# Kernel tuning notes

Hardware: AMD Instinct MI355X
Metric: run time of the kernel (lower is better)

Reference implementation:

```python
import jax, jax.numpy as jnp
import numpy as np

BN_EPS = 1e-5
L2_EPS = 1e-12
REG = 10.0      # 'reg' inside ProxRefinement.forward
LAMBDA = 0.1    # Softshrink lambd (reg=0.1 in ProxRefinement.__init__)
STEPS = 10
LR = 0.01


def _softshrink(x, lam):
    return jnp.where(x > lam, x - lam, jnp.where(x < -lam, x + lam, jnp.zeros_like(x)))


def _batched_graphsage(x, adj, W, b, gamma, beta):
    # x: [B,N,F_in], adj: [B,N,N], W: [F_out,F_in]
    h = jnp.einsum('bnm,bmf->bnf', adj, x)            # neighborhood aggregate
    h = jnp.einsum('bnf,of->bno', h, W) + b           # Linear
    norm = jnp.linalg.norm(h, axis=2, keepdims=True)  # F.normalize(dim=2, p=2)
    h = h / jnp.maximum(norm, L2_EPS)
    h = jax.nn.relu(h)
    # BatchNorm1d(num_features=N) in training mode: stats over (batch, feature)
    mu = h.mean(axis=(0, 2))
    var = h.var(axis=(0, 2))
    h = (h - mu[None, :, None]) / jnp.sqrt(var[None, :, None] + BN_EPS)
    return h * gamma[None, :, None] + beta[None, :, None]


def _prox_refine(s, lap):
    s0 = s

    def body(_, s):
        grad = (jnp.einsum('bmn,bmk->bnk', lap, s)   # lap^T @ s
                + jnp.einsum('bnm,bmk->bnk', lap, s)  # lap @ s
                - REG * 2.0 * (s0 - s))
        return _softshrink(s - LR * grad, LAMBDA)

    return jax.lax.fori_loop(0, STEPS, body, s)


def setup_inputs() -> dict:
    key = jax.random.key(0)
    ks = jax.random.split(key, 6)
    B, N, nfeat, nnext = 8, 2048, 256, 512
    nhid = nfeat // 2
    x = jax.random.normal(ks[0], (B, N, nfeat), dtype=jnp.float32)
    adj = jax.random.uniform(ks[1], (B, N, N), dtype=jnp.float32)
    W1 = jax.random.normal(ks[2], (nhid, nfeat), dtype=jnp.float32) * (1.0 / np.sqrt(nfeat))
    b1 = jnp.zeros((nhid,), dtype=jnp.float32)
    g1 = jnp.ones((N,), dtype=jnp.float32)
    be1 = jnp.zeros((N,), dtype=jnp.float32)
    W2 = jax.random.normal(ks[3], (nnext, nhid), dtype=jnp.float32) * (1.0 / np.sqrt(nhid))
    b2 = jnp.zeros((nnext,), dtype=jnp.float32)
    g2 = jnp.ones((N,), dtype=jnp.float32)
    be2 = jnp.zeros((N,), dtype=jnp.float32)
    return {"x": x, "adj": adj, "W1": W1, "b1": b1, "g1": g1, "be1": be1,
            "W2": W2, "b2": b2, "g2": g2, "be2": be2}


def reference(x, adj, W1, b1, g1, be1, W2, b2, g2, be2):
    s = _batched_graphsage(x, adj, W1, b1, g1, be1)   # [B,N,nhid]
    s = _batched_graphsage(s, adj, W2, b2, g2, be2)   # [B,N,nnext]
    # Laplacian L = diag(rowsum(adj)) - adj, vectorized over batch
    deg = adj.sum(axis=-1)                             # [B,N]
    N = adj.shape[1]
    lap = deg[:, :, None] * jnp.eye(N, dtype=adj.dtype)[None] - adj
    s = _prox_refine(s, lap)
    return jax.nn.softmax(s, axis=-1)
```

## Files before the change

### kernel.cpp

```cpp
#include <hip/hip_runtime.h>
#include <cstdint>
#include <cstddef>

#define NN 2048
#define NB 8
#define F0C 256
#define F1C 128
#define F2C 512

typedef double f64x4 __attribute__((ext_vector_type(4)));

__device__ __forceinline__ double waveSumD(double v) {
#pragma unroll
    for (int o = 32; o; o >>= 1) v += __shfl_down(v, o, 64);
    return v;
}

__global__ __launch_bounds__(256) void deg_k(const float* __restrict__ adj,
                                             double* __restrict__ degD) {
    const size_t row = blockIdx.x;
    const float4* r4 = (const float4*)(adj + row * (size_t)NN);
    float4 a = r4[threadIdx.x];
    float4 b = r4[threadIdx.x + 256];
    double s = (((double)a.x + a.y) + ((double)a.z + a.w)) +
               (((double)b.x + b.y) + ((double)b.z + b.w));
    s = waveSumD(s);
    __shared__ double red[4];
    if (!(threadIdx.x & 63)) red[threadIdx.x >> 6] = s;
    __syncthreads();
    if (!threadIdx.x) degD[row] = (red[0] + red[1]) + (red[2] + red[3]);
}

template <typename BT, typename CT, bool ADD_AT, int EPI>
__global__ __launch_bounds__(256, 2) void mf_k(
    const float* __restrict__ A, size_t Abatch, int lda,
    const BT* __restrict__ Bm, size_t Bbatch, int ldb,
    CT* __restrict__ Cout, size_t Cbatch, int K, int Ccols,
    const float* __restrict__ S0, size_t Sbatch,
    const double* __restrict__ degD) {
    __shared__ float As[128][20];
    __shared__ float AsT[ADD_AT ? 16 : 1][136];
    __shared__ BT Bs[16][132];
    __shared__ double degL[EPI == 2 ? 128 : 1];

    const int b = blockIdx.z;
    const int i0 = blockIdx.x * 128;
    const int j0 = blockIdx.y * 128;
    const float* Ab = A + Abatch * (size_t)b;
    const BT* Bb = Bm + Bbatch * (size_t)b;
    const int t = threadIdx.x;
    const int l = t & 63;
    const int wv = t >> 6;
    const int wr = (wv >> 1) * 64;
    const int wc = (wv & 1) * 64;
    const int lr = l & 15;
    const int lk = l >> 4;

    f64x4 acc[4][4];
#pragma unroll
    for (int r = 0; r < 4; ++r)
#pragma unroll
        for (int c = 0; c < 4; ++c)
#pragma unroll
            for (int v = 0; v < 4; ++v) acc[r][c][v] = 0.0;

    if (EPI == 2) {
        if (t < 128) degL[t] = degD[(size_t)b * NN + i0 + t];
    }

    for (int k0 = 0; k0 < K; k0 += 16) {
        if (k0) __syncthreads();
#pragma unroll
        for (int r2 = 0; r2 < 2; ++r2) {
            const int p = t + 256 * r2;
            const int i = p >> 2, q = p & 3;
            float4 v = *(const float4*)(Ab + (size_t)(i0 + i) * lda + k0 + q * 4);
            *(float4*)&As[i][q * 4] = v;
        }
        if (ADD_AT) {
#pragma unroll
            for (int r2 = 0; r2 < 2; ++r2) {
                const int p = t + 256 * r2;
                const int k = p >> 5, c = (p & 31) * 4;
                float4 v = *(const float4*)(Ab + (size_t)(k0 + k) * lda + i0 + c);
                *(float4*)&AsT[k][c] = v;
            }
        }
        if constexpr (sizeof(BT) == 8) {
#pragma unroll
            for (int r2 = 0; r2 < 2; ++r2) {
                const int p = t + 256 * r2;
                const int k = p >> 5, c = (p & 31) * 4;
                const BT* src = Bb + (size_t)(k0 + k) * ldb + j0 + c;
                double2 u0 = *(const double2*)src;
                double2 u1 = *(const double2*)(src + 2);
                *(double2*)&Bs[k][c] = u0;
                *(double2*)&Bs[k][c + 2] = u1;
            }
        } else {
#pragma unroll
            for (int r2 = 0; r2 < 2; ++r2) {
                const int p = t + 256 * r2;
                const int k = p >> 5, c = (p & 31) * 4;
                float4 v = *(const float4*)(Bb + (size_t)(k0 + k) * ldb + j0 + c);
                Bs[k][c + 0] = (BT)v.x; Bs[k][c + 1] = (BT)v.y;
                Bs[k][c + 2] = (BT)v.z; Bs[k][c + 3] = (BT)v.w;
            }
        }
        __syncthreads();
#pragma unroll
        for (int kk = 0; kk < 4; ++kk) {
            const int kr = kk * 4 + lk;
            double av[4], bv[4];
#pragma unroll
            for (int r = 0; r < 4; ++r) {
                const int ii = wr + r * 16 + lr;
                double a = (double)As[ii][kr];
                if (ADD_AT) a += (double)AsT[kr][ii];
                av[r] = a;
            }
#pragma unroll
            for (int c = 0; c < 4; ++c)
                bv[c] = (double)Bs[kr][wc + c * 16 + lr];
#pragma unroll
            for (int r = 0; r < 4; ++r)
#pragma unroll
                for (int c = 0; c < 4; ++c)
                    acc[r][c] = __builtin_amdgcn_mfma_f64_16x16x4f64(
                        av[r], bv[c], acc[r][c], 0, 0, 0);
        }
    }

#pragma unroll
    for (int r = 0; r < 4; ++r) {
#pragma unroll
        for (int v = 0; v < 4; ++v) {
            const int rl = wr + r * 16 + lk + 4 * v;
            const size_t grow = (size_t)(i0 + rl);
            double cA = 0.0;
            if (EPI == 2) cA = 0.8 - 0.02 * degL[rl];
#pragma unroll
            for (int c = 0; c < 4; ++c) {
                const int gcol = j0 + wc + c * 16 + lr;
                double y = acc[r][c][v];
                if (EPI == 2) {
                    const double sv = (double)Bb[grow * (size_t)ldb + gcol];
                    const double s0v =
                        (double)S0[Sbatch * (size_t)b + grow * (size_t)Ccols + gcol];
                    const double u = cA * sv + 0.01 * y + 0.2 * s0v;
                    y = (u > 0.1) ? (u - 0.1) : ((u < -0.1) ? (u + 0.1) : 0.0);
                }
                Cout[Cbatch * (size_t)b + grow * (size_t)Ccols + gcol] = (CT)y;
            }
        }
    }
}

template <typename BT, typename CT>
__global__ __launch_bounds__(256) void gemm64_k(
    const float* __restrict__ A, size_t Abatch, int lda,
    const BT* __restrict__ Bm, size_t Bbatch, int ldb,
    CT* __restrict__ Cout, size_t Cbatch,
    int K, int Ccols,
    const float* __restrict__ bias,
    const float* __restrict__ S0, size_t Sbatch,
    int addAT, int btrans, int epi) {
    __shared__ float As[32][132];
    __shared__ float AsT[32][132];
    __shared__ BT Bs[32][68];
    __shared__ double degLDS[2][128];
    const int b = blockIdx.z;
    const int i0 = blockIdx.x * 128;
    const int j0 = blockIdx.y * 64;
    const float* Ab = A + Abatch * (size_t)b;
    const BT* Bb = Bm + Bbatch * (size_t)b;
    const int t = threadIdx.x;
    const int wv = t >> 6, ln = t & 63;
    const int ri = (wv >> 1) * 64 + (ln >> 3) * 8;
    const int rj = ((wv & 1) * 8 + (ln & 7)) * 4;

    double acc[8][4];
#pragma unroll
    for (int i = 0; i < 8; ++i)
#pragma unroll
        for (int j = 0; j < 4; ++j) acc[i][j] = 0.0;

    const int a_i = t >> 1, a_m = (t & 1) * 16;
    const int p_m = t >> 3, p_i = (t & 7) * 16;
    const int b_m = t >> 3, b_j = (t & 7) * 8;
    const int w_j = t >> 2, w_m = (t & 3) * 8;
    double degacc = 0.0;

    for (int k0 = 0; k0 < K; k0 += 32) {
        if (k0) __syncthreads();
        {
            const float4* src =
                (const float4*)(Ab + (size_t)(i0 + a_i) * lda + k0 + a_m);
            float4 v0 = src[0], v1 = src[1], v2 = src[2], v3 = src[3];
            if (epi == 2)
                degacc += (((double)v0.x + v0.y) + ((double)v0.z + v0.w)) +
                          (((double)v1.x + v1.y) + ((double)v1.z + v1.w)) +
                          (((double)v2.x + v2.y) + ((double)v2.z + v2.w)) +
                          (((double)v3.x + v3.y) + ((double)v3.z + v3.w));
            As[a_m + 0][a_i] = v0.x;  As[a_m + 1][a_i] = v0.y;
            As[a_m + 2][a_i] = v0.z;  As[a_m + 3][a_i] = v0.w;
            As[a_m + 4][a_i] = v1.x;  As[a_m + 5][a_i] = v1.y;
            As[a_m + 6][a_i] = v1.z;  As[a_m + 7][a_i] = v1.w;
            As[a_m + 8][a_i] = v2.x;  As[a_m + 9][a_i] = v2.y;
            As[a_m + 10][a_i] = v2.z; As[a_m + 11][a_i] = v2.w;
            As[a_m + 12][a_i] = v3.x; As[a_m + 13][a_i] = v3.y;
            As[a_m + 14][a_i] = v3.z; As[a_m + 15][a_i] = v3.w;
        }
        if (addAT) {
            const float4* src =
                (const float4*)(Ab + (size_t)(k0 + p_m) * lda + i0 + p_i);
            float4 v0 = src[0], v1 = src[1], v2 = src[2], v3 = src[3];
            AsT[p_m][p_i + 0] = v0.x;  AsT[p_m][p_i + 1] = v0.y;
            AsT[p_m][p_i + 2] = v0.z;  AsT[p_m][p_i + 3] = v0.w;
            AsT[p_m][p_i + 4] = v1.x;  AsT[p_m][p_i + 5] = v1.y;
            AsT[p_m][p_i + 6] = v1.z;  AsT[p_m][p_i + 7] = v1.w;
            AsT[p_m][p_i + 8] = v2.x;  AsT[p_m][p_i + 9] = v2.y;
            AsT[p_m][p_i + 10] = v2.z; AsT[p_m][p_i + 11] = v2.w;
            AsT[p_m][p_i + 12] = v3.x; AsT[p_m][p_i + 13] = v3.y;
            AsT[p_m][p_i + 14] = v3.z; AsT[p_m][p_i + 15] = v3.w;
        }
        if (!btrans) {
            const BT* src = Bb + (size_t)(k0 + b_m) * ldb + j0 + b_j;
            if constexpr (sizeof(BT) == 8) {
                const double2* s2 = (const double2*)src;
                double2 u0 = s2[0], u1 = s2[1], u2 = s2[2], u3 = s2[3];
                Bs[b_m][b_j + 0] = (BT)u0.x; Bs[b_m][b_j + 1] = (BT)u0.y;
                Bs[b_m][b_j + 2] = (BT)u1.x; Bs[b_m][b_j + 3] = (BT)u1.y;
                Bs[b_m][b_j + 4] = (BT)u2.x; Bs[b_m][b_j + 5] = (BT)u2.y;
                Bs[b_m][b_j + 6] = (BT)u3.x; Bs[b_m][b_j + 7] = (BT)u3.y;
            } else {
                const float4* s4 = (const float4*)src;
                float4 u0 = s4[0], u1 = s4[1];
                Bs[b_m][b_j + 0] = (BT)u0.x; Bs[b_m][b_j + 1] = (BT)u0.y;
                Bs[b_m][b_j + 2] = (BT)u0.z; Bs[b_m][b_j + 3] = (BT)u0.w;
                Bs[b_m][b_j + 4] = (BT)u1.x; Bs[b_m][b_j + 5] = (BT)u1.y;
                Bs[b_m][b_j + 6] = (BT)u1.z; Bs[b_m][b_j + 7] = (BT)u1.w;
            }
        } else {
            const float* Wf = reinterpret_cast<const float*>(Bm);
            const float4* src =
                (const float4*)(Wf + (size_t)(j0 + w_j) * ldb + k0 + w_m);
            float4 v0 = src[0], v1 = src[1];
            Bs[w_m + 0][w_j] = (BT)v0.x; Bs[w_m + 1][w_j] = (BT)v0.y;
            Bs[w_m + 2][w_j] = (BT)v0.z; Bs[w_m + 3][w_j] = (BT)v0.w;
            Bs[w_m + 4][w_j] = (BT)v1.x; Bs[w_m + 5][w_j] = (BT)v1.y;
            Bs[w_m + 6][w_j] = (BT)v1.z; Bs[w_m + 7][w_j] = (BT)v1.w;
        }
        __syncthreads();
#pragma unroll 4
        for (int mk = 0; mk < 32; ++mk) {
            float4 a0 = *(const float4*)&As[mk][ri];
            float4 a1 = *(const float4*)&As[mk][ri + 4];
            double ad[8] = {a0.x, a0.y, a0.z, a0.w, a1.x, a1.y, a1.z, a1.w};
            if (addAT) {
                float4 t0 = *(const float4*)&AsT[mk][ri];
                float4 t1 = *(const float4*)&AsT[mk][ri + 4];
                ad[0] += t0.x; ad[1] += t0.y; ad[2] += t0.z; ad[3] += t0.w;
                ad[4] += t1.x; ad[5] += t1.y; ad[6] += t1.z; ad[7] += t1.w;
            }
            double bd[4];
#pragma unroll
            for (int c = 0; c < 4; ++c) bd[c] = (double)Bs[mk][rj + c];
#pragma unroll
            for (int iy = 0; iy < 8; ++iy)
#pragma unroll
                for (int jx = 0; jx < 4; ++jx)
                    acc[iy][jx] = fma(ad[iy], bd[jx], acc[iy][jx]);
        }
    }

    if (epi == 2) degLDS[t & 1][t >> 1] = degacc;
    __syncthreads();

#pragma unroll
    for (int iy = 0; iy < 8; ++iy) {
        const int row = i0 + ri + iy;
        CT* cp = Cout + Cbatch * (size_t)b + (size_t)row * Ccols + j0 + rj;
        CT o[4];
        if (epi == 0) {
#pragma unroll
            for (int jx = 0; jx < 4; ++jx) o[jx] = (CT)acc[iy][jx];
        } else if (epi == 1) {
#pragma unroll
            for (int jx = 0; jx < 4; ++jx)
                o[jx] = (CT)(acc[iy][jx] + (double)bias[j0 + rj + jx]);
        } else {
            const double dg = degLDS[0][ri + iy] + degLDS[1][ri + iy];
            const double cA = 0.8 - 0.02 * dg;
            const BT* sp = Bb + (size_t)row * ldb + j0 + rj;
            const float* s0p = S0 + Sbatch * (size_t)b + (size_t)row * Ccols + j0 + rj;
#pragma unroll
            for (int jx = 0; jx < 4; ++jx) {
                const double u = cA * (double)sp[jx] + 0.01 * acc[iy][jx] +
                                 0.2 * (double)s0p[jx];
                const double v = (u > 0.1) ? (u - 0.1) : ((u < -0.1) ? (u + 0.1) : 0.0);
                o[jx] = (CT)v;
            }
        }
        if constexpr (sizeof(CT) == 8) {
            double2 q0, q1;
            q0.x = o[0]; q0.y = o[1]; q1.x = o[2]; q1.y = o[3];
            *(double2*)cp = q0;
            *(double2*)(cp + 2) = q1;
        } else {
            *(float4*)cp = make_float4(o[0], o[1], o[2], o[3]);
        }
    }
}

__global__ __launch_bounds__(64) void l2relu_k(float* __restrict__ buf, int F) {
    const size_t row = blockIdx.x;
    float* p = buf + row * (size_t)F;
    double ss = 0.0;
    for (int k = threadIdx.x; k < F; k += 64) {
        const double v = (double)p[k];
        ss += v * v;
    }
#pragma unroll
    for (int o = 32; o; o >>= 1) ss += __shfl_xor(ss, o, 64);
    const double den = fmax(sqrt(ss), 1e-12);
    for (int k = threadIdx.x; k < F; k += 64) {
        const double v = (double)p[k] / den;
        p[k] = (float)(v > 0.0 ? v : 0.0);
    }
}

__global__ __launch_bounds__(256) void bn_k(float* __restrict__ buf,
                                            const float* __restrict__ g,
                                            const float* __restrict__ be, int fl) {
    const int n = blockIdx.x;
    const int F = 1 << fl;
    const int total = NB << fl;
    __shared__ double red[4];
    __shared__ double sh_m, sh_scale, sh_be;
    const int wv = threadIdx.x >> 6, ln = threadIdx.x & 63;
    double s = 0.0;
    for (int idx = threadIdx.x; idx < total; idx += 256) {
        const int bb = idx >> fl, f = idx & (F - 1);
        s += (double)buf[((size_t)bb * NN + n) * F + f];
    }
    s = waveSumD(s);
    if (!ln) red[wv] = s;
    __syncthreads();
    if (!threadIdx.x) sh_m = ((red[0] + red[1]) + (red[2] + red[3])) / (double)total;
    __syncthreads();
    const double m = sh_m;
    double v2 = 0.0;
    for (int idx = threadIdx.x; idx < total; idx += 256) {
        const int bb = idx >> fl, f = idx & (F - 1);
        const double d = (double)buf[((size_t)bb * NN + n) * F + f] - m;
        v2 += d * d;
    }
    v2 = waveSumD(v2);
    __syncthreads();
    if (!ln) red[wv] = v2;
    __syncthreads();
    if (!threadIdx.x) {
        const double var = ((red[0] + red[1]) + (red[2] + red[3])) / (double)total;
        sh_scale = (1.0 / sqrt(var + 1e-5)) * (double)g[n];
        sh_be = (double)be[n];
    }
    __syncthreads();
    const double sc = sh_scale, bb2 = sh_be;
    for (int idx = threadIdx.x; idx < total; idx += 256) {
        const int bb = idx >> fl, f = idx & (F - 1);
        float* pp = &buf[((size_t)bb * NN + n) * F + f];
        *pp = (float)(((double)*pp - m) * sc + bb2);
    }
}

template <typename T>
__global__ __launch_bounds__(256) void softmax_k(const T* __restrict__ in,
                                                 float* __restrict__ out) {
    const size_t row = blockIdx.x;
    const T* p = in + row * (size_t)F2C;
    float* q = out + row * (size_t)F2C;
    const int t = threadIdx.x;
    const int wv = t >> 6, ln = t & 63;
    const double v0 = (double)p[t], v1 = (double)p[t + 256];
    double m = fmax(v0, v1);
#pragma unroll
    for (int o = 32; o; o >>= 1) m = fmax(m, __shfl_xor(m, o, 64));
    __shared__ double red[4];
    if (!ln) red[wv] = m;
    __syncthreads();
    m = fmax(fmax(red[0], red[1]), fmax(red[2], red[3]));
    const double e0 = exp(v0 - m), e1 = exp(v1 - m);
    double s = e0 + e1;
#pragma unroll
    for (int o = 32; o; o >>= 1) s += __shfl_xor(s, o, 64);
    __syncthreads();
    if (!ln) red[wv] = s;
    __syncthreads();
    s = (red[0] + red[1]) + (red[2] + red[3]);
    q[t] = (float)(e0 / s);
    q[t + 256] = (float)(e1 / s);
}

extern "C" void kernel_launch(void* const* d_in, const int* in_sizes, int n_in,
                              void* d_out, int out_size, void* d_ws, size_t ws_size,
                              hipStream_t stream) {
    const float* x = (const float*)d_in[0];
    const float* adj = (const float*)d_in[1];
    const float* W1 = (const float*)d_in[2];
    const float* b1 = (const float*)d_in[3];
    const float* g1 = (const float*)d_in[4];
    const float* be1 = (const float*)d_in[5];
    const float* W2 = (const float*)d_in[6];
    const float* b2 = (const float*)d_in[7];
    const float* g2 = (const float*)d_in[8];
    const float* be2 = (const float*)d_in[9];
    float* out = (float*)d_out;
    float* ws = (float*)d_ws;

    const size_t M2 = (size_t)NB * NN * F2C;
    const size_t szAgg = (size_t)NB * NN * F0C;

    const int tier = (ws_size >= ((size_t)192 << 20)) ? 0
                   : (ws_size >= ((size_t)64 << 20)) ? 1 : 2;

    if (tier == 0) {
        float* s0F = ws;
        float* tmpF = ws + M2;
        double* D1 = (double*)(ws + 2 * M2);
        double* D2 = D1 + M2;
        float* aggF = tmpF;
        float* t1F = tmpF + szAgg;
        float* h2F = tmpF;
        double* degD = (double*)(tmpF + 7340032);

        deg_k<<<NB * NN, 256, 0, stream>>>(adj, degD);
        mf_k<float, float, false, 0><<<dim3(16, 2, 8), 256, 0, stream>>>(
            adj, (size_t)NN * NN, NN, x, (size_t)NN * F0C, F0C,
            aggF, (size_t)NN * F0C, NN, F0C, nullptr, 0, nullptr);
        gemm64_k<float, float><<<dim3(128, 2, 1), 256, 0, stream>>>(
            aggF, 0, F0C, W1, 0, F0C, t1F, 0, F0C, F1C, b1, nullptr, 0, 0, 1, 1);
        l2relu_k<<<NB * NN, 64, 0, stream>>>(t1F, F1C);
        bn_k<<<NN, 256, 0, stream>>>(t1F, g1, be1, 7);
        mf_k<float, float, false, 0><<<dim3(16, 1, 8), 256, 0, stream>>>(
            adj, (size_t)NN * NN, NN, t1F, (size_t)NN * F1C, F1C,
            h2F, (size_t)NN * F1C, NN, F1C, nullptr, 0, nullptr);
        gemm64_k<float, float><<<dim3(128, 8, 1), 256, 0, stream>>>(
            h2F, 0, F1C, W2, 0, F1C, s0F, 0, F1C, F2C, b2, nullptr, 0, 0, 1, 1);
        l2relu_k<<<NB * NN, 64, 0, stream>>>(s0F, F2C);
        bn_k<<<NN, 256, 0, stream>>>(s0F, g2, be2, 9);
        mf_k<float, double, true, 2><<<dim3(16, 4, 8), 256, 0, stream>>>(
            adj, (size_t)NN * NN, NN, s0F, (size_t)NN * F2C, F2C,
            D1, (size_t)NN * F2C, NN, F2C, s0F, (size_t)NN * F2C, degD);
        const double* Sin = D1;
        for (int it = 1; it < 10; ++it) {
            double* Sout = (it & 1) ? D2 : D1;
            mf_k<double, double, true, 2><<<dim3(16, 4, 8), 256, 0, stream>>>(
                adj, (size_t)NN * NN, NN, Sin, (size_t)NN * F2C, F2C,
                Sout, (size_t)NN * F2C, NN, F2C, s0F, (size_t)NN * F2C, degD);
            Sin = Sout;
        }
        softmax_k<double><<<NB * NN, 256, 0, stream>>>(D2, out);
    } else if (tier == 1) {
        float* R0 = ws;
        float* R1 = ws + M2;
        float* aggF = R1;
        float* t1F = R0;
        float* h2F = R1;
        float* s0F = R0;

        gemm64_k<float, float><<<dim3(16, 4, 8), 256, 0, stream>>>(
            adj, (size_t)NN * NN, NN, x, (size_t)NN * F0C, F0C,
            aggF, (size_t)NN * F0C, NN, F0C, nullptr, nullptr, 0, 0, 0, 0);
        gemm64_k<float, float><<<dim3(128, 2, 1), 256, 0, stream>>>(
            aggF, 0, F0C, W1, 0, F0C, t1F, 0, F0C, F1C, b1, nullptr, 0, 0, 1, 1);
        l2relu_k<<<NB * NN, 64, 0, stream>>>(t1F, F1C);
        bn_k<<<NN, 256, 0, stream>>>(t1F, g1, be1, 7);
        gemm64_k<float, float><<<dim3(16, 2, 8), 256, 0, stream>>>(
            adj, (size_t)NN * NN, NN, t1F, (size_t)NN * F1C, F1C,
            h2F, (size_t)NN * F1C, NN, F1C, nullptr, nullptr, 0, 0, 0, 0);
        gemm64_k<float, float><<<dim3(128, 8, 1), 256, 0, stream>>>(
            h2F, 0, F1C, W2, 0, F1C, s0F, 0, F1C, F2C, b2, nullptr, 0, 0, 1, 1);
        l2relu_k<<<NB * NN, 64, 0, stream>>>(s0F, F2C);
        bn_k<<<NN, 256, 0, stream>>>(s0F, g2, be2, 9);
        const float* Sin = s0F;
        for (int it = 0; it < 10; ++it) {
            float* Sout = (it & 1) ? out : R1;
            gemm64_k<float, float><<<dim3(16, 8, 8), 256, 0, stream>>>(
                adj, (size_t)NN * NN, NN, Sin, (size_t)NN * F2C, F2C,
                Sout, (size_t)NN * F2C, NN, F2C, nullptr, s0F, (size_t)NN * F2C, 1, 0, 2);
            Sin = Sout;
        }
        softmax_k<float><<<NB * NN, 256, 0, stream>>>(out, out);
    } else {
        float* Wp0 = ws;
        float* Wp1 = ws + (size_t)NN * F2C;
        float* xW1 = ws;
        float* t1 = out;
        float* h2 = ws;
        float* s0 = out;

        gemm64_k<float, float><<<dim3(128, 2, 1), 256, 0, stream>>>(
            x, 0, F0C, W1, 0, F0C, xW1, 0, F0C, F1C, nullptr, nullptr, 0, 0, 1, 0);
        gemm64_k<float, float><<<dim3(16, 2, 8), 256, 0, stream>>>(
            adj, (size_t)NN * NN, NN, xW1, (size_t)NN * F1C, F1C,
            t1, (size_t)NN * F1C, NN, F1C, b1, nullptr, 0, 0, 0, 1);
        l2relu_k<<<NB * NN, 64, 0, stream>>>(t1, F1C);
        bn_k<<<NN, 256, 0, stream>>>(t1, g1, be1, 7);
        gemm64_k<float, float><<<dim3(16, 2, 8), 256, 0, stream>>>(
            adj, (size_t)NN * NN, NN, t1, (size_t)NN * F1C, F1C,
            h2, (size_t)NN * F1C, NN, F1C, nullptr, nullptr, 0, 0, 0, 0);
        gemm64_k<float, float><<<dim3(128, 8, 1), 256, 0, stream>>>(
            h2, 0, F1C, W2, 0, F1C, s0, 0, F1C, F2C, b2, nullptr, 0, 0, 1, 1);
        l2relu_k<<<NB * NN, 64, 0, stream>>>(s0, F2C);
        bn_k<<<NN, 256, 0, stream>>>(s0, g2, be2, 9);
        for (int b = 0; b < NB; ++b) {
            float* s0b = out + (size_t)b * NN * F2C;
            const float* Ab = adj + (size_t)b * NN * NN;
            const float* Sin = s0b;
            for (int it = 0; it < 10; ++it) {
                float* Sout = (it == 9) ? s0b : ((it & 1) ? Wp1 : Wp0);
                gemm64_k<float, float><<<dim3(16, 8, 1), 256, 0, stream>>>(
                    Ab, 0, NN, Sin, 0, F2C,
                    Sout, 0, NN, F2C, nullptr, s0b, 0, 1, 0, 2);
                Sin = Sout;
            }
        }
        softmax_k<float><<<NB * NN, 256, 0, stream>>>(out, out);
    }
}
```

Measured before the change: 6.990 ms.

## Double-buffer LDS tiles with register prefetch in the FP64 MFMA GEMM

The GEMM kernel now keeps two LDS buffers for the A, A-transpose and B tiles. It loads the next K-slice from global memory into registers while the MFMAs run on the current slice, then writes those registers into the other buffer. The goal is to hide global load latency behind compute and to drop one of the two barriers per K step. The cost is roughly double the shared memory and extra registers for the prefetched data, which could limit occupancy at two blocks per CU.

```diff
diff --git a/kernel.cpp b/kernel.cpp
--- a/kernel.cpp
+++ b/kernel.cpp
@@ -38,9 +38,9 @@
     CT* __restrict__ Cout, size_t Cbatch, int K, int Ccols,
     const float* __restrict__ S0, size_t Sbatch,
     const double* __restrict__ degD) {
-    __shared__ float As[128][20];
-    __shared__ float AsT[ADD_AT ? 16 : 1][136];
-    __shared__ BT Bs[16][132];
+    __shared__ float As[2][128][20];
+    __shared__ float AsT[2][ADD_AT ? 16 : 1][136];
+    __shared__ BT Bs[2][16][132];
     __shared__ double degL[EPI == 2 ? 128 : 1];
 
     const int b = blockIdx.z;
@@ -56,6 +56,74 @@
     const int lr = l & 15;
     const int lk = l >> 4;
 
+    const int sa_i = t >> 2, sa_q = (t & 3) * 4;
+    const int st_k = t >> 4, st_c = (t & 15) * 4;
+    const int sb_k = t >> 5, sb_c = (t & 31) * 4;
+
+    float4 aR[2];
+    float4 atR[2];
+    double2 bRd[2][2];
+    float4 bRf[2];
+
+    auto LOAD = [&](int k0) {
+#pragma unroll
+        for (int r2 = 0; r2 < 2; ++r2) {
+            const int i = sa_i + 64 * r2;
+            aR[r2] = *(const float4*)(Ab + (size_t)(i0 + i) * lda + k0 + sa_q);
+        }
+        if (ADD_AT) {
+#pragma unroll
+            for (int r2 = 0; r2 < 2; ++r2) {
+                const int k = sb_k + 8 * r2;
+                atR[r2] = *(const float4*)(Ab + (size_t)(k0 + k) * lda + i0 + sb_c);
+            }
+        }
+        if constexpr (sizeof(BT) == 8) {
+#pragma unroll
+            for (int r2 = 0; r2 < 2; ++r2) {
+                const int k = sb_k + 8 * r2;
+                const BT* src = Bb + (size_t)(k0 + k) * ldb + j0 + sb_c;
+                bRd[r2][0] = *(const double2*)src;
+                bRd[r2][1] = *(const double2*)(src + 2);
+            }
+        } else {
+#pragma unroll
+            for (int r2 = 0; r2 < 2; ++r2) {
+                const int k = sb_k + 8 * r2;
+                bRf[r2] = *(const float4*)(Bb + (size_t)(k0 + k) * ldb + j0 + sb_c);
+            }
+        }
+    };
+
+    auto STORE = [&](int bf) {
+#pragma unroll
+        for (int r2 = 0; r2 < 2; ++r2) {
+            const int i = sa_i + 64 * r2;
+            *(float4*)&As[bf][i][sa_q] = aR[r2];
+        }
+        if (ADD_AT) {
+#pragma unroll
+            for (int r2 = 0; r2 < 2; ++r2) {
+                const int k = sb_k + 8 * r2;
+                *(float4*)&AsT[bf][k][sb_c] = atR[r2];
+            }
+        }
+        if constexpr (sizeof(BT) == 8) {
+#pragma unroll
+            for (int r2 = 0; r2 < 2; ++r2) {
+                const int k = sb_k + 8 * r2;
+                *(double2*)&Bs[bf][k][sb_c] = bRd[r2][0];
+                *(double2*)&Bs[bf][k][sb_c + 2] = bRd[r2][1];
+            }
+        } else {
+#pragma unroll
+            for (int r2 = 0; r2 < 2; ++r2) {
+                const int k = sb_k + 8 * r2;
+                *(float4*)&Bs[bf][k][sb_c] = bRf[r2];
+            }
+        }
+    };
+
     f64x4 acc[4][4];
 #pragma unroll
     for (int r = 0; r < 4; ++r)
@@ -68,46 +136,14 @@
         if (t < 128) degL[t] = degD[(size_t)b * NN + i0 + t];
     }
 
-    for (int k0 = 0; k0 < K; k0 += 16) {
-        if (k0) __syncthreads();
-#pragma unroll
-        for (int r2 = 0; r2 < 2; ++r2) {
-            const int p = t + 256 * r2;
-            const int i = p >> 2, q = p & 3;
-            float4 v = *(const float4*)(Ab + (size_t)(i0 + i) * lda + k0 + q * 4);
-            *(float4*)&As[i][q * 4] = v;
-        }
-        if (ADD_AT) {
-#pragma unroll
-            for (int r2 = 0; r2 < 2; ++r2) {
-                const int p = t + 256 * r2;
-                const int k = p >> 5, c = (p & 31) * 4;
-                float4 v = *(const float4*)(Ab + (size_t)(k0 + k) * lda + i0 + c);
-                *(float4*)&AsT[k][c] = v;
-            }
-        }
-        if constexpr (sizeof(BT) == 8) {
-#pragma unroll
-            for (int r2 = 0; r2 < 2; ++r2) {
-                const int p = t + 256 * r2;
-                const int k = p >> 5, c = (p & 31) * 4;
-                const BT* src = Bb + (size_t)(k0 + k) * ldb + j0 + c;
-                double2 u0 = *(const double2*)src;
-                double2 u1 = *(const double2*)(src + 2);
-                *(double2*)&Bs[k][c] = u0;
-                *(double2*)&Bs[k][c + 2] = u1;
-            }
-        } else {
-#pragma unroll
-            for (int r2 = 0; r2 < 2; ++r2) {
-                const int p = t + 256 * r2;
-                const int k = p >> 5, c = (p & 31) * 4;
-                float4 v = *(const float4*)(Bb + (size_t)(k0 + k) * ldb + j0 + c);
-                Bs[k][c + 0] = (BT)v.x; Bs[k][c + 1] = (BT)v.y;
-                Bs[k][c + 2] = (BT)v.z; Bs[k][c + 3] = (BT)v.w;
-            }
-        }
-        __syncthreads();
+    const int nk = K / 16;
+    LOAD(0);
+    STORE(0);
+    __syncthreads();
+
+    for (int ks = 0; ks < nk; ++ks) {
+        const int cur = ks & 1;
+        if (ks + 1 < nk) LOAD((ks + 1) * 16);
 #pragma unroll
         for (int kk = 0; kk < 4; ++kk) {
             const int kr = kk * 4 + lk;
@@ -115,19 +151,23 @@
 #pragma unroll
             for (int r = 0; r < 4; ++r) {
                 const int ii = wr + r * 16 + lr;
-                double a = (double)As[ii][kr];
-                if (ADD_AT) a += (double)AsT[kr][ii];
+                double a = (double)As[cur][ii][kr];
+                if (ADD_AT) a += (double)AsT[cur][kr][ii];
                 av[r] = a;
             }
 #pragma unroll
             for (int c = 0; c < 4; ++c)
-                bv[c] = (double)Bs[kr][wc + c * 16 + lr];
+                bv[c] = (double)Bs[cur][kr][wc + c * 16 + lr];
 #pragma unroll
             for (int r = 0; r < 4; ++r)
 #pragma unroll
                 for (int c = 0; c < 4; ++c)
                     acc[r][c] = __builtin_amdgcn_mfma_f64_16x16x4f64(
                         av[r], bv[c], acc[r][c], 0, 0, 0);
+        }
+        if (ks + 1 < nk) {
+            STORE(cur ^ 1);
+            __syncthreads();
         }
     }
 
```

Result: slower. 8.117 ms (+16.1%).

## Double-buffer shared-memory tiles with register prefetch in MFMA GEMM kernel

Applied to the files above, without the earlier changes.

The templated fp64 MFMA GEMM kernel now keeps two shared-memory buffers for the A, A-transpose and B tiles. While MFMAs run on the current buffer, the next k-slice is loaded from global memory into registers. The loop is unrolled by two and needs one barrier per k-step instead of two. This is meant to hide global-load latency behind compute, at the cost of twice the LDS footprint, more registers, and an assumption that K/16 is even.

```diff
diff --git a/kernel.cpp b/kernel.cpp
--- a/kernel.cpp
+++ b/kernel.cpp
@@ -38,9 +38,9 @@
     CT* __restrict__ Cout, size_t Cbatch, int K, int Ccols,
     const float* __restrict__ S0, size_t Sbatch,
     const double* __restrict__ degD) {
-    __shared__ float As[128][20];
-    __shared__ float AsT[ADD_AT ? 16 : 1][136];
-    __shared__ BT Bs[16][132];
+    __shared__ float As[2][128][20];
+    __shared__ float AsT[2][ADD_AT ? 16 : 1][136];
+    __shared__ BT Bs[2][16][132];
     __shared__ double degL[EPI == 2 ? 128 : 1];
 
     const int b = blockIdx.z;
@@ -56,6 +56,78 @@
     const int lr = l & 15;
     const int lk = l >> 4;
 
+    const int sa_i = t >> 2, sa_q = (t & 3) * 4;
+    const int sb_k = t >> 5, sb_c = (t & 31) * 4;
+
+    float4 aR0, aR1;
+    float4 tR0, tR1;
+    double2 bD0, bD1, bD2, bD3;
+    float4 bF0, bF1;
+
+#define MF_LOAD(K0)                                                              \
+    {                                                                            \
+        const int _k0 = (K0);                                                    \
+        aR0 = *(const float4*)(Ab + (size_t)(i0 + sa_i) * lda + _k0 + sa_q);     \
+        aR1 = *(const float4*)(Ab + (size_t)(i0 + sa_i + 64) * lda + _k0 + sa_q);\
+        if constexpr (ADD_AT) {                                                  \
+            tR0 = *(const float4*)(Ab + (size_t)(_k0 + sb_k) * lda + i0 + sb_c); \
+            tR1 = *(const float4*)(Ab + (size_t)(_k0 + sb_k + 8) * lda + i0 + sb_c);\
+        }                                                                        \
+        if constexpr (sizeof(BT) == 8) {                                         \
+            const BT* _s0 = Bb + (size_t)(_k0 + sb_k) * ldb + j0 + sb_c;         \
+            const BT* _s1 = Bb + (size_t)(_k0 + sb_k + 8) * ldb + j0 + sb_c;     \
+            bD0 = *(const double2*)_s0; bD1 = *(const double2*)(_s0 + 2);        \
+            bD2 = *(const double2*)_s1; bD3 = *(const double2*)(_s1 + 2);        \
+        } else {                                                                 \
+            bF0 = *(const float4*)(Bb + (size_t)(_k0 + sb_k) * ldb + j0 + sb_c); \
+            bF1 = *(const float4*)(Bb + (size_t)(_k0 + sb_k + 8) * ldb + j0 + sb_c);\
+        }                                                                        \
+    }
+
+#define MF_STORE(BF)                                                             \
+    {                                                                            \
+        *(float4*)&As[BF][sa_i][sa_q] = aR0;                                     \
+        *(float4*)&As[BF][sa_i + 64][sa_q] = aR1;                                \
+        if constexpr (ADD_AT) {                                                  \
+            *(float4*)&AsT[BF][sb_k][sb_c] = tR0;                                \
+            *(float4*)&AsT[BF][sb_k + 8][sb_c] = tR1;                            \
+        }                                                                        \
+        if constexpr (sizeof(BT) == 8) {                                         \
+            *(double2*)&Bs[BF][sb_k][sb_c] = bD0;                                \
+            *(double2*)&Bs[BF][sb_k][sb_c + 2] = bD1;                            \
+            *(double2*)&Bs[BF][sb_k + 8][sb_c] = bD2;                            \
+            *(double2*)&Bs[BF][sb_k + 8][sb_c + 2] = bD3;                        \
+        } else {                                                                 \
+            *(float4*)&Bs[BF][sb_k][sb_c] = bF0;                                 \
+            *(float4*)&Bs[BF][sb_k + 8][sb_c] = bF1;                             \
+        }                                                                        \
+    }
+
+#define MF_COMP(CUR)                                                             \
+    {                                                                            \
+        _Pragma("unroll")                                                        \
+        for (int kk = 0; kk < 4; ++kk) {                                         \
+            const int kr = kk * 4 + lk;                                          \
+            double av[4], bv[4];                                                 \
+            _Pragma("unroll")                                                    \
+            for (int r = 0; r < 4; ++r) {                                        \
+                const int ii = wr + r * 16 + lr;                                 \
+                double a = (double)As[CUR][ii][kr];                              \
+                if constexpr (ADD_AT) a += (double)AsT[CUR][kr][ii];             \
+                av[r] = a;                                                       \
+            }                                                                    \
+            _Pragma("unroll")                                                    \
+            for (int c = 0; c < 4; ++c)                                          \
+                bv[c] = (double)Bs[CUR][kr][wc + c * 16 + lr];                   \
+            _Pragma("unroll")                                                    \
+            for (int r = 0; r < 4; ++r)                                          \
+                _Pragma("unroll")                                                \
+                for (int c = 0; c < 4; ++c)                                      \
+                    acc[r][c] = __builtin_amdgcn_mfma_f64_16x16x4f64(            \
+                        av[r], bv[c], acc[r][c], 0, 0, 0);                       \
+        }                                                                        \
+    }
+
     f64x4 acc[4][4];
 #pragma unroll
     for (int r = 0; r < 4; ++r)
@@ -68,68 +140,26 @@
         if (t < 128) degL[t] = degD[(size_t)b * NN + i0 + t];
     }
 
-    for (int k0 = 0; k0 < K; k0 += 16) {
-        if (k0) __syncthreads();
-#pragma unroll
-        for (int r2 = 0; r2 < 2; ++r2) {
-            const int p = t + 256 * r2;
-            const int i = p >> 2, q = p & 3;
-            float4 v = *(const float4*)(Ab + (size_t)(i0 + i) * lda + k0 + q * 4);
-            *(float4*)&As[i][q * 4] = v;
-        }
-        if (ADD_AT) {
-#pragma unroll
-            for (int r2 = 0; r2 < 2; ++r2) {
-                const int p = t + 256 * r2;
-                const int k = p >> 5, c = (p & 31) * 4;
-                float4 v = *(const float4*)(Ab + (size_t)(k0 + k) * lda + i0 + c);
-                *(float4*)&AsT[k][c] = v;
-            }
-        }
-        if constexpr (sizeof(BT) == 8) {
-#pragma unroll
-            for (int r2 = 0; r2 < 2; ++r2) {
-                const int p = t + 256 * r2;
-                const int k = p >> 5, c = (p & 31) * 4;
-                const BT* src = Bb + (size_t)(k0 + k) * ldb + j0 + c;
-                double2 u0 = *(const double2*)src;
-                double2 u1 = *(const double2*)(src + 2);
-                *(double2*)&Bs[k][c] = u0;
-                *(double2*)&Bs[k][c + 2] = u1;
-            }
-        } else {
-#pragma unroll
-            for (int r2 = 0; r2 < 2; ++r2) {
-                const int p = t + 256 * r2;
-                const int k = p >> 5, c = (p & 31) * 4;
-                float4 v = *(const float4*)(Bb + (size_t)(k0 + k) * ldb + j0 + c);
-                Bs[k][c + 0] = (BT)v.x; Bs[k][c + 1] = (BT)v.y;
-                Bs[k][c + 2] = (BT)v.z; Bs[k][c + 3] = (BT)v.w;
-            }
-        }
+    const int nk = K / 16;
+    MF_LOAD(0);
+    MF_STORE(0);
+    __syncthreads();
+
+    for (int ks = 0; ks < nk; ks += 2) {
+        MF_LOAD((ks + 1) * 16);
+        MF_COMP(0);
+        MF_STORE(1);
         __syncthreads();
-#pragma unroll
-        for (int kk = 0; kk < 4; ++kk) {
-            const int kr = kk * 4 + lk;
-            double av[4], bv[4];
-#pragma unroll
-            for (int r = 0; r < 4; ++r) {
-                const int ii = wr + r * 16 + lr;
-                double a = (double)As[ii][kr];
-                if (ADD_AT) a += (double)AsT[kr][ii];
-                av[r] = a;
-            }
-#pragma unroll
-            for (int c = 0; c < 4; ++c)
-                bv[c] = (double)Bs[kr][wc + c * 16 + lr];
-#pragma unroll
-            for (int r = 0; r < 4; ++r)
-#pragma unroll
-                for (int c = 0; c < 4; ++c)
-                    acc[r][c] = __builtin_amdgcn_mfma_f64_16x16x4f64(
-                        av[r], bv[c], acc[r][c], 0, 0, 0);
-        }
-    }
+        if (ks + 2 < nk) MF_LOAD((ks + 2) * 16);
+        MF_COMP(1);
+        if (ks + 2 < nk) {
+            MF_STORE(0);
+            __syncthreads();
+        }
+    }
+#undef MF_LOAD
+#undef MF_STORE
+#undef MF_COMP
 
 #pragma unroll
     for (int r = 0; r < 4; ++r) {
```

Measured after the change: 6.444 ms. 7.8% less time.
